# Kernel tuning notes

Measured on AMD Instinct MI355X. Metric: run time of the kernel, lower is better.

Reference implementation:

```python
import jax, jax.numpy as jnp
import numpy as np

B, D, H, T, S, FD = 4, 1024, 12, 32, 32, 64
NUM_BUCKETS = 32
MAX_BUCKET = NUM_BUCKETS // 2            # 16
MIN_BUCKET = MAX_BUCKET - NUM_BUCKETS + 1  # -15


def setup_inputs() -> dict:
    key = jax.random.key(0)
    k1, k2, k3 = jax.random.split(key, 3)
    qk = jax.random.normal(k1, (B, D, H, T, FD), dtype=jnp.float32)
    # raw (unclamped) pairwise frame distances, exercises both clamp bounds
    pairwise_distances = jax.random.randint(k2, (B, T, S), -40, 40, dtype=jnp.int32)
    lookup_table_weight = jax.random.normal(k3, (NUM_BUCKETS, H, FD), dtype=jnp.float32) * 0.02
    return {"qk": qk, "pairwise_distances": pairwise_distances,
            "lookup_table_weight": lookup_table_weight}


def reference(qk, pairwise_distances, lookup_table_weight):
    # clamp distances to bucket range [MIN_BUCKET, MAX_BUCKET]
    pd = jnp.clip(pairwise_distances, MIN_BUCKET, MAX_BUCKET)
    # torch negative indexing wraps: idx in [0, NUM_BUCKETS)
    idx = jnp.where(pd < 0, pd + NUM_BUCKETS, pd)
    R = lookup_table_weight[idx]  # [B, T, S, H, F]
    # mode == 'qk': per-(b,t,s) dot of qk features with gathered RPE vectors
    return jnp.einsum('bdhtf,btshf->bdhts', qk, R)  # [B, D, H, T, S]
```

## Files before the change

### kernel.cpp

```cpp
#include <hip/hip_runtime.h>
#include <hip/hip_bf16.h>

constexpr int Bc = 4, Dc = 1024, Hc = 12, Tc = 32, Sc = 32, Fc = 64;
constexpr int QD = Hc * Tc * Fc;
constexpr int OD = Hc * Tc * Sc;
constexpr int DCH = 16;

typedef __bf16 bf16x8 __attribute__((ext_vector_type(8)));
typedef float  f32x4  __attribute__((ext_vector_type(4)));

__global__ __launch_bounds__(256) void rpe_mfma(
    const float* __restrict__ qk,
    const int*   __restrict__ pdist,
    const float* __restrict__ lut,
    float*       __restrict__ out)
{
    __shared__ __bf16        Rl[32][72];
    __shared__ unsigned char idxl[Tc][Sc];

    const int bid = blockIdx.x;
    const int dc  = bid & 63;
    int tmp = bid >> 6;
    const int h = tmp % Hc;
    const int b = tmp / Hc;
    const int d0 = dc * DCH;

    const int tid = threadIdx.x;

    {
        const int bu = tid >> 3;
        const int f0 = (tid & 7) * 8;
        const float* lp = lut + (bu * Hc + h) * Fc + f0;
        f32x4 v0 = *reinterpret_cast<const f32x4*>(lp);
        f32x4 v1 = *reinterpret_cast<const f32x4*>(lp + 4);
        bf16x8 w;
        #pragma unroll
        for (int j = 0; j < 4; ++j) { w[j] = (__bf16)v0[j]; w[j + 4] = (__bf16)v1[j]; }
        *reinterpret_cast<bf16x8*>(&Rl[bu][f0]) = w;
    }
    {
        const int t  = tid >> 3;
        const int s0 = (tid & 7) * 4;
        const int4 p = *reinterpret_cast<const int4*>(
            pdist + (b * Tc + t) * Sc + s0);
        uchar4 u;
        int v;
        v = p.x; v = v < -15 ? -15 : (v > 16 ? 16 : v); u.x = (unsigned char)(v < 0 ? v + 32 : v);
        v = p.y; v = v < -15 ? -15 : (v > 16 ? 16 : v); u.y = (unsigned char)(v < 0 ? v + 32 : v);
        v = p.z; v = v < -15 ? -15 : (v > 16 ? 16 : v); u.z = (unsigned char)(v < 0 ? v + 32 : v);
        v = p.w; v = v < -15 ? -15 : (v > 16 ? 16 : v); u.w = (unsigned char)(v < 0 ? v + 32 : v);
        *reinterpret_cast<uchar4*>(&idxl[t][s0]) = u;
    }
    __syncthreads();

    const int lane = tid & 63;
    const int wv   = tid >> 6;
    const int r16  = lane & 15;
    const int grp  = lane >> 4;

    const float* qb = qk  + ((size_t)(b * Dc + d0 + r16) * Hc + h) * Tc * Fc + grp * 8;
    float*       ob = out + ((size_t)(b * Dc + d0 + r16) * Hc + h) * Tc * Sc;

    #pragma unroll 2
    for (int i = 0; i < 8; ++i) {
        const int t = wv * 8 + i;

        const int i0 = idxl[t][r16];
        const int i1 = idxl[t][16 + r16];
        bf16x8 a00 = *reinterpret_cast<const bf16x8*>(&Rl[i0][grp * 8]);
        bf16x8 a01 = *reinterpret_cast<const bf16x8*>(&Rl[i0][32 + grp * 8]);
        bf16x8 a10 = *reinterpret_cast<const bf16x8*>(&Rl[i1][grp * 8]);
        bf16x8 a11 = *reinterpret_cast<const bf16x8*>(&Rl[i1][32 + grp * 8]);

        const float* qr = qb + t * Fc;
        f32x4 q0 = *reinterpret_cast<const f32x4*>(qr);
        f32x4 q1 = *reinterpret_cast<const f32x4*>(qr + 4);
        f32x4 q2 = *reinterpret_cast<const f32x4*>(qr + 32);
        f32x4 q3 = *reinterpret_cast<const f32x4*>(qr + 36);
        bf16x8 bf0, bf1;
        #pragma unroll
        for (int j = 0; j < 4; ++j) {
            bf0[j] = (__bf16)q0[j]; bf0[j + 4] = (__bf16)q1[j];
            bf1[j] = (__bf16)q2[j]; bf1[j + 4] = (__bf16)q3[j];
        }

        f32x4 acc0 = {0.f, 0.f, 0.f, 0.f};
        f32x4 acc1 = {0.f, 0.f, 0.f, 0.f};
        acc0 = __builtin_amdgcn_mfma_f32_16x16x32_bf16(a00, bf0, acc0, 0, 0, 0);
        acc0 = __builtin_amdgcn_mfma_f32_16x16x32_bf16(a01, bf1, acc0, 0, 0, 0);
        acc1 = __builtin_amdgcn_mfma_f32_16x16x32_bf16(a10, bf0, acc1, 0, 0, 0);
        acc1 = __builtin_amdgcn_mfma_f32_16x16x32_bf16(a11, bf1, acc1, 0, 0, 0);

        float* op = ob + t * Sc;
        *reinterpret_cast<f32x4*>(op + grp * 4)      = acc0;
        *reinterpret_cast<f32x4*>(op + 16 + grp * 4) = acc1;
    }
}

extern "C" void kernel_launch(void* const* d_in, const int* in_sizes, int n_in,
                              void* d_out, int out_size, void* d_ws, size_t ws_size,
                              hipStream_t stream) {
    const float* qk    = (const float*)d_in[0];
    const int*   pdist = (const int*)d_in[1];
    const float* lut   = (const float*)d_in[2];
    float*       out   = (float*)d_out;

    const int grid = Bc * Hc * (Dc / DCH);
    rpe_mfma<<<grid, 256, 0, stream>>>(qk, pdist, lut, out);
}
```

Measured before the change: 131.0 us.

## Stage qk through double-buffered LDS with coalesced loads across heads per block

Each block of 512 threads now handles six heads for a 16-row d-chunk. Each step loads the next half-head's qk slice with fully coalesced reads, converts it to bf16 and stores it into a double-buffered shared-memory tile while the MFMAs run on the current tile. The LUT slice is staged per head in the same way. This replaces the strided per-lane global qk loads and cuts the grid to 512 blocks. In exchange it adds a barrier every step, more registers for prefetch, and much more LDS per block, which may lower occupancy.

```diff
diff --git a/kernel.cpp b/kernel.cpp
--- a/kernel.cpp
+++ b/kernel.cpp
@@ -2,54 +2,75 @@
 #include <hip/hip_bf16.h>
 
 constexpr int Bc = 4, Dc = 1024, Hc = 12, Tc = 32, Sc = 32, Fc = 64;
-constexpr int QD = Hc * Tc * Fc;
-constexpr int OD = Hc * Tc * Sc;
 constexpr int DCH = 16;
+constexpr int HB  = 6;
+constexpr int STEPS = 2 * HB;
+constexpr int QPITCH = 1032;
 
 typedef __bf16 bf16x8 __attribute__((ext_vector_type(8)));
+typedef __bf16 bf16x4 __attribute__((ext_vector_type(4)));
 typedef float  f32x4  __attribute__((ext_vector_type(4)));
 
-__global__ __launch_bounds__(256) void rpe_mfma(
+__global__ __launch_bounds__(512, 4) void rpe_staged(
     const float* __restrict__ qk,
     const int*   __restrict__ pdist,
     const float* __restrict__ lut,
     float*       __restrict__ out)
 {
-    __shared__ __bf16        Rl[32][72];
+    __shared__ __align__(16) __bf16 Qs[2][DCH][QPITCH];
+    __shared__ __align__(16) __bf16 Rl[2][32][72];
     __shared__ unsigned char idxl[Tc][Sc];
 
     const int bid = blockIdx.x;
-    const int dc  = bid & 63;
-    int tmp = bid >> 6;
-    const int h = tmp % Hc;
-    const int b = tmp / Hc;
-    const int d0 = dc * DCH;
+    const int hh  = bid & 1;
+    const int dc  = (bid >> 1) & 63;
+    const int b   = bid >> 7;
+    const int d0  = dc * DCH;
+    const int h0  = hh * HB;
 
     const int tid = threadIdx.x;
 
-    {
-        const int bu = tid >> 3;
-        const int f0 = (tid & 7) * 8;
-        const float* lp = lut + (bu * Hc + h) * Fc + f0;
-        f32x4 v0 = *reinterpret_cast<const f32x4*>(lp);
-        f32x4 v1 = *reinterpret_cast<const f32x4*>(lp + 4);
-        bf16x8 w;
-        #pragma unroll
-        for (int j = 0; j < 4; ++j) { w[j] = (__bf16)v0[j]; w[j + 4] = (__bf16)v1[j]; }
-        *reinterpret_cast<bf16x8*>(&Rl[bu][f0]) = w;
-    }
-    {
+    const int sd = tid >> 5;
+    const int sc = tid & 31;
+    const float* qsrc = qk + (size_t)((b * Dc + d0 + sd) * Hc) * Tc * Fc + sc * 8;
+
+    const int rbu = tid >> 4;
+    const int rf0 = (tid & 15) * 4;
+
+    if (tid < 256) {
         const int t  = tid >> 3;
         const int s0 = (tid & 7) * 4;
-        const int4 p = *reinterpret_cast<const int4*>(
-            pdist + (b * Tc + t) * Sc + s0);
-        uchar4 u;
-        int v;
+        const int4 p = *reinterpret_cast<const int4*>(pdist + (b * Tc + t) * Sc + s0);
+        uchar4 u; int v;
         v = p.x; v = v < -15 ? -15 : (v > 16 ? 16 : v); u.x = (unsigned char)(v < 0 ? v + 32 : v);
         v = p.y; v = v < -15 ? -15 : (v > 16 ? 16 : v); u.y = (unsigned char)(v < 0 ? v + 32 : v);
         v = p.z; v = v < -15 ? -15 : (v > 16 ? 16 : v); u.z = (unsigned char)(v < 0 ? v + 32 : v);
         v = p.w; v = v < -15 ? -15 : (v > 16 ? 16 : v); u.w = (unsigned char)(v < 0 ? v + 32 : v);
         *reinterpret_cast<uchar4*>(&idxl[t][s0]) = u;
+    }
+    f32x4 g[4][2];
+    f32x4 rg;
+    {
+        const float* qp = qsrc + h0 * 2048;
+        #pragma unroll
+        for (int j = 0; j < 4; ++j) {
+            g[j][0] = *reinterpret_cast<const f32x4*>(qp + j * 256);
+            g[j][1] = *reinterpret_cast<const f32x4*>(qp + j * 256 + 4);
+        }
+        rg = *reinterpret_cast<const f32x4*>(lut + (rbu * Hc + h0) * Fc + rf0);
+    }
+    #pragma unroll
+    for (int j = 0; j < 4; ++j) {
+        bf16x8 w;
+        #pragma unroll
+        for (int k = 0; k < 4; ++k) { w[k] = (__bf16)g[j][0][k]; w[k + 4] = (__bf16)g[j][1][k]; }
+        *reinterpret_cast<bf16x8*>(&Qs[0][sd][sc * 8 + j * 256]) = w;
+    }
+    {
+        bf16x4 w4;
+        #pragma unroll
+        for (int k = 0; k < 4; ++k) w4[k] = (__bf16)rg[k];
+        *reinterpret_cast<bf16x4*>(&Rl[0][rbu][rf0]) = w4;
     }
     __syncthreads();
 
@@ -57,43 +78,68 @@
     const int wv   = tid >> 6;
     const int r16  = lane & 15;
     const int grp  = lane >> 4;
-
-    const float* qb = qk  + ((size_t)(b * Dc + d0 + r16) * Hc + h) * Tc * Fc + grp * 8;
-    float*       ob = out + ((size_t)(b * Dc + d0 + r16) * Hc + h) * Tc * Sc;
+    float* obase = out + (size_t)((b * Dc + d0 + r16) * Hc) * Tc * Sc;
 
     #pragma unroll 2
-    for (int i = 0; i < 8; ++i) {
-        const int t = wv * 8 + i;
+    for (int s = 0; s < STEPS; ++s) {
+        const int buf   = s & 1;
+        const int hl    = s >> 1;
+        const int thalf = s & 1;
+        const int h     = h0 + hl;
 
-        const int i0 = idxl[t][r16];
-        const int i1 = idxl[t][16 + r16];
-        bf16x8 a00 = *reinterpret_cast<const bf16x8*>(&Rl[i0][grp * 8]);
-        bf16x8 a01 = *reinterpret_cast<const bf16x8*>(&Rl[i0][32 + grp * 8]);
-        bf16x8 a10 = *reinterpret_cast<const bf16x8*>(&Rl[i1][grp * 8]);
-        bf16x8 a11 = *reinterpret_cast<const bf16x8*>(&Rl[i1][32 + grp * 8]);
-
-        const float* qr = qb + t * Fc;
-        f32x4 q0 = *reinterpret_cast<const f32x4*>(qr);
-        f32x4 q1 = *reinterpret_cast<const f32x4*>(qr + 4);
-        f32x4 q2 = *reinterpret_cast<const f32x4*>(qr + 32);
-        f32x4 q3 = *reinterpret_cast<const f32x4*>(qr + 36);
-        bf16x8 bf0, bf1;
-        #pragma unroll
-        for (int j = 0; j < 4; ++j) {
-            bf0[j] = (__bf16)q0[j]; bf0[j + 4] = (__bf16)q1[j];
-            bf1[j] = (__bf16)q2[j]; bf1[j + 4] = (__bf16)q3[j];
+        if (s + 1 < STEPS) {
+            const float* qp = qsrc + (h0 + ((s + 1) >> 1)) * 2048 + ((s + 1) & 1) * 1024;
+            #pragma unroll
+            for (int j = 0; j < 4; ++j) {
+                g[j][0] = *reinterpret_cast<const f32x4*>(qp + j * 256);
+                g[j][1] = *reinterpret_cast<const f32x4*>(qp + j * 256 + 4);
+            }
+            if (s & 1)
+                rg = *reinterpret_cast<const f32x4*>(
+                    lut + (rbu * Hc + h0 + ((s + 1) >> 1)) * Fc + rf0);
         }
 
-        f32x4 acc0 = {0.f, 0.f, 0.f, 0.f};
-        f32x4 acc1 = {0.f, 0.f, 0.f, 0.f};
-        acc0 = __builtin_amdgcn_mfma_f32_16x16x32_bf16(a00, bf0, acc0, 0, 0, 0);
-        acc0 = __builtin_amdgcn_mfma_f32_16x16x32_bf16(a01, bf1, acc0, 0, 0, 0);
-        acc1 = __builtin_amdgcn_mfma_f32_16x16x32_bf16(a10, bf0, acc1, 0, 0, 0);
-        acc1 = __builtin_amdgcn_mfma_f32_16x16x32_bf16(a11, bf1, acc1, 0, 0, 0);
+        #pragma unroll
+        for (int tt = 0; tt < 2; ++tt) {
+            const int tl = wv * 2 + tt;
+            const int tg = thalf * 16 + tl;
+            const int i0 = idxl[tg][r16];
+            const int i1 = idxl[tg][16 + r16];
+            bf16x8 a00 = *reinterpret_cast<const bf16x8*>(&Rl[hl & 1][i0][grp * 8]);
+            bf16x8 a01 = *reinterpret_cast<const bf16x8*>(&Rl[hl & 1][i0][32 + grp * 8]);
+            bf16x8 a10 = *reinterpret_cast<const bf16x8*>(&Rl[hl & 1][i1][grp * 8]);
+            bf16x8 a11 = *reinterpret_cast<const bf16x8*>(&Rl[hl & 1][i1][32 + grp * 8]);
+            bf16x8 bf0 = *reinterpret_cast<const bf16x8*>(&Qs[buf][r16][tl * 64 + grp * 8]);
+            bf16x8 bf1 = *reinterpret_cast<const bf16x8*>(&Qs[buf][r16][tl * 64 + 32 + grp * 8]);
 
-        float* op = ob + t * Sc;
-        *reinterpret_cast<f32x4*>(op + grp * 4)      = acc0;
-        *reinterpret_cast<f32x4*>(op + 16 + grp * 4) = acc1;
+            f32x4 acc0 = {0.f, 0.f, 0.f, 0.f};
+            f32x4 acc1 = {0.f, 0.f, 0.f, 0.f};
+            acc0 = __builtin_amdgcn_mfma_f32_16x16x32_bf16(a00, bf0, acc0, 0, 0, 0);
+            acc0 = __builtin_amdgcn_mfma_f32_16x16x32_bf16(a01, bf1, acc0, 0, 0, 0);
+            acc1 = __builtin_amdgcn_mfma_f32_16x16x32_bf16(a10, bf0, acc1, 0, 0, 0);
+            acc1 = __builtin_amdgcn_mfma_f32_16x16x32_bf16(a11, bf1, acc1, 0, 0, 0);
+
+            float* op = obase + h * (Tc * Sc) + tg * Sc;
+            *reinterpret_cast<f32x4*>(op + grp * 4)      = acc0;
+            *reinterpret_cast<f32x4*>(op + 16 + grp * 4) = acc1;
+        }
+
+        if (s + 1 < STEPS) {
+            #pragma unroll
+            for (int j = 0; j < 4; ++j) {
+                bf16x8 w;
+                #pragma unroll
+                for (int k = 0; k < 4; ++k) { w[k] = (__bf16)g[j][0][k]; w[k + 4] = (__bf16)g[j][1][k]; }
+                *reinterpret_cast<bf16x8*>(&Qs[buf ^ 1][sd][sc * 8 + j * 256]) = w;
+            }
+            if (s & 1) {
+                bf16x4 w4;
+                #pragma unroll
+                for (int k = 0; k < 4; ++k) w4[k] = (__bf16)rg[k];
+                *reinterpret_cast<bf16x4*>(&Rl[((s + 1) >> 1) & 1][rbu][rf0]) = w4;
+            }
+        }
+        __syncthreads();
     }
 }
 
@@ -105,6 +151,6 @@
     const float* lut   = (const float*)d_in[2];
     float*       out   = (float*)d_out;
 
-    const int grid = Bc * Hc * (Dc / DCH);
-    rpe_mfma<<<grid, 256, 0, stream>>>(qk, pdist, lut, out);
+    const int grid = Bc * 64 * 2;
+    rpe_staged<<<grid, 512, 0, stream>>>(qk, pdist, lut, out);
 }
```

Measured after the change: 124.8 us. 1.05x faster.
